# Performance work log

Hardware: AMD Instinct MI355X
Metric: run time of the kernel (lower is better)

## Reference

```python
import jax, jax.numpy as jnp
import numpy as np
import math

POWER = 4
NUM_LEVELS = 2
STDS = [8, 4, 2, 1]          # stds sorted descending, as in __init__
KSIZE = 31                    # max(stds)*4 - 1
MAX_MIP = (NUM_LEVELS - 1) + math.log(2 * max(STDS)) / math.log(POWER)  # 3.0


def _blur_kernel():
    # (12, 3, 31, 31): output channel 3*i+c is a Gaussian(std=STDS[i]) applied to input channel c
    d = np.arange(KSIZE, dtype=np.float64) - (KSIZE - 1) / 2.0
    K = np.zeros((3 * len(STDS), 3, KSIZE, KSIZE), np.float32)
    for i, s in enumerate(STDS):
        g1 = np.exp(-0.5 * (d / s) ** 2)
        g1 = g1 / g1.sum()
        g = np.outer(g1, g1).astype(np.float32)
        for c in range(3):
            K[3 * i + c, c] = g
    return jnp.asarray(K)


def cube_sample(tex, dirs):
    # tex: (6, H, W, 3) cubemap faces in OpenGL order (+x,-x,+y,-y,+z,-z); dirs: (B, 3)
    H, W = tex.shape[1], tex.shape[2]
    x, y, z = dirs[:, 0], dirs[:, 1], dirs[:, 2]
    ax, ay, az = jnp.abs(x), jnp.abs(y), jnp.abs(z)
    is_x = (ax >= ay) & (ax >= az)
    is_y = (~is_x) & (ay >= az)
    face = jnp.where(is_x, jnp.where(x >= 0, 0, 1),
                     jnp.where(is_y, jnp.where(y >= 0, 2, 3),
                               jnp.where(z >= 0, 4, 5)))
    ma = jnp.where(is_x, ax, jnp.where(is_y, ay, az))
    conds = [face == i for i in range(6)]
    sc = jnp.select(conds, [-z, z, x, x, x, -x])
    tc = jnp.select(conds, [-y, -y, z, -z, -y, -y])
    inv = 1.0 / jnp.maximum(ma, 1e-12)
    u = 0.5 * (sc * inv + 1.0)
    v = 0.5 * (tc * inv + 1.0)
    fx = u * W - 0.5
    fy = v * H - 0.5
    x0 = jnp.floor(fx)
    y0 = jnp.floor(fy)
    wx = (fx - x0)[:, None]
    wy = (fy - y0)[:, None]
    x0i = jnp.clip(x0, 0, W - 1).astype(jnp.int32)
    x1i = jnp.clip(x0 + 1, 0, W - 1).astype(jnp.int32)
    y0i = jnp.clip(y0, 0, H - 1).astype(jnp.int32)
    y1i = jnp.clip(y0 + 1, 0, H - 1).astype(jnp.int32)
    t00 = tex[face, y0i, x0i]
    t10 = tex[face, y0i, x1i]
    t01 = tex[face, y1i, x0i]
    t11 = tex[face, y1i, x1i]
    return ((t00 * (1 - wx) + t10 * wx) * (1 - wy)
            + (t01 * (1 - wx) + t11 * wx) * wy)


def setup_inputs() -> dict:
    key = jax.random.key(0)
    k1, k2, k3, k4 = jax.random.split(key, 4)
    B = 2097152
    res = 512
    viewdirs = jax.random.normal(k1, (B, 3), dtype=jnp.float32)
    viewdirs = viewdirs / jnp.linalg.norm(viewdirs, axis=-1, keepdims=True)
    # miplevel = log(saSample/saTexel)/log(4)/2 ; make it span [0, 3.2] so the mask path fires
    saTexel = 4.0 * math.pi / (6 * res * res)
    u = jax.random.uniform(k2, (B, 1), dtype=jnp.float32)
    saSample = saTexel * (float(POWER) ** (2.0 * 3.2 * u))
    # learned cubemaps: coarse (128) then fine (512), as in bg_mats list order
    bg_mat0 = 0.1 + 0.05 * jax.random.normal(k3, (6, 128, 128, 3), dtype=jnp.float32)
    bg_mat1 = 0.1 + 0.05 * jax.random.normal(k4, (6, 512, 512, 3), dtype=jnp.float32)
    return {"viewdirs": viewdirs, "saSample": saSample, "bg_mat0": bg_mat0, "bg_mat1": bg_mat1}


def reference(viewdirs, saSample, bg_mat0, bg_mat1):
    res = bg_mat1.shape[1]
    saTexel = 4.0 * math.pi / (6 * res * res)
    miplevel = jnp.clip(jnp.log(saSample / saTexel) / math.log(POWER) / 2.0, 0.0, MAX_MIP)  # (B,1)

    # main level pass: mip=1 (coarse, weight 1/(2-1)=1), mip=0 (fine, weight 1/2)
    img = cube_sample(bg_mat0, viewdirs) * 1.0 + cube_sample(bg_mat1, viewdirs) * 0.5

    # blur pyramid from coarse map (start_mip=1, weight=1, identity activation)
    faces = jnp.transpose(bg_mat0, (0, 3, 1, 2))  # (6,3,h,h)
    conv = jax.lax.conv_general_dilated(faces, _blur_kernel(), (1, 1), 'SAME',
                                        dimension_numbers=('NCHW', 'OIHW', 'NCHW'))
    blur = jnp.zeros_like(img)
    wsum = jnp.zeros_like(miplevel)
    for i, s in enumerate(STDS):
        mat = jnp.transpose(conv[:, 3 * i:3 * i + 3], (0, 2, 3, 1))  # (6,h,h,3)
        mip = (NUM_LEVELS - 1) + math.log(2 * s) / math.log(POWER)
        w = 1.0 - jnp.clip(jnp.abs(mip - miplevel), 0.0, 1.0)  # (B,1)
        blur = blur + cube_sample(mat, viewdirs) * w
        wsum = wsum + w
    mask = miplevel >= NUM_LEVELS  # (B,1)
    img = jnp.where(mask, blur / jnp.maximum(wsum, 1e-8), img)
    return img
```

## Files before the change

kernel.cpp:

```cpp
#include <hip/hip_runtime.h>
#include <hip/hip_fp16.h>
#include <math.h>

#define KSIZE 31
#define HRAD 15

#define QSCALE (1023.0f / 0.75f)
#define QINV   (0.75f / 1023.0f)
#define QOFF   0.25f

union H8U { float4 f4; __half h[8]; };

__device__ inline unsigned quant3(float r, float g, float b) {
    int qr = (int)((r + QOFF) * QSCALE + 0.5f);
    int qg = (int)((g + QOFF) * QSCALE + 0.5f);
    int qb = (int)((b + QOFF) * QSCALE + 0.5f);
    qr = min(max(qr, 0), 1023);
    qg = min(max(qg, 0), 1023);
    qb = min(max(qb, 0), 1023);
    return (unsigned)(qr | (qg << 10) | (qb << 20));
}

__device__ inline float deqc(unsigned q, int sh) {
    return (float)((q >> sh) & 1023u) * QINV - QOFF;
}

__device__ inline void cube_coords(float x, float y, float z,
                                   int& face, float& u, float& v) {
    float ax = fabsf(x), ay = fabsf(y), az = fabsf(z);
    bool is_x = (ax >= ay) && (ax >= az);
    bool is_y = (!is_x) && (ay >= az);
    float ma, sc, tc;
    if (is_x) {
        if (x >= 0.0f) { face = 0; sc = -z; } else { face = 1; sc = z; }
        ma = ax; tc = -y;
    } else if (is_y) {
        if (y >= 0.0f) { face = 2; tc = z; } else { face = 3; tc = -z; }
        ma = ay; sc = x;
    } else {
        if (z >= 0.0f) { face = 4; sc = x; } else { face = 5; sc = -x; }
        ma = az; tc = -y;
    }
    float inv = 1.0f / fmaxf(ma, 1e-12f);
    u = 0.5f * (sc * inv + 1.0f);
    v = 0.5f * (tc * inv + 1.0f);
}

__device__ inline void nbq_setup(float u, float v, int HW, int face,
                                 int& rec, float& wx, float& wy) {
    float fx = u * (float)HW - 0.5f;
    float fy = v * (float)HW - 0.5f;
    float x0 = floorf(fx), y0 = floorf(fy);
    wx = fx - x0;
    wy = fy - y0;
    int xi = (int)x0, yi = (int)y0;
    if (xi < 0) { xi = 0; wx = 0.0f; }
    if (yi < 0) { yi = 0; wy = 0.0f; }
    rec = (face * HW + yi) * HW + xi;
}

__device__ inline void weights_inline(int tid, float wS[4][32]) {
    const float ss[4] = {8.f, 4.f, 2.f, 1.f};
    int lvl = (tid >> 5) & 3;
    int tap = tid & 31;
    float d = (float)tap - 15.0f;
    float q = d / ss[lvl];
    float g = (tap < KSIZE) ? expf(-0.5f * q * q) : 0.0f;
    float s = g;
#pragma unroll
    for (int k = 16; k; k >>= 1) s += __shfl_xor(s, k, 32);
    if (tid < 128) wS[lvl][tap] = g / s;
}

__global__ __launch_bounds__(256)
void hblur(const float* __restrict__ bg0, float4* __restrict__ tmpH,
           uint4* __restrict__ bg0q) {
    __shared__ float sm[1664];
    float (*rows)[2][384] = (float (*)[2][384])sm;
    float (*wS)[32] = (float (*)[32])(sm + 1536);

    int bid  = blockIdx.x;
    int tid  = threadIdx.x;
    int unit = tid >> 7;
    int lane = tid & 127;
    int face = bid / 64;
    int yrow = (bid % 64) * 2 + unit;

    weights_inline(tid, wS);

    int ynext = min(yrow + 1, 127);
    const float* srcA = bg0 + (size_t)(face * 128 + yrow) * 384;
    const float* srcB = bg0 + (size_t)(face * 128 + ynext) * 384;
    for (int k = lane; k < 384; k += 128) {
        rows[unit][0][k] = srcA[k];
        rows[unit][1][k] = srcB[k];
    }
    __syncthreads();

    int x = lane;
    float a[4][3] = {};
    for (int t = 0; t < KSIZE; ++t) {
        int xx = x + t - HRAD;
        if (xx >= 0 && xx < 128) {
            float r0 = rows[unit][0][xx * 3 + 0];
            float r1 = rows[unit][0][xx * 3 + 1];
            float r2 = rows[unit][0][xx * 3 + 2];
#pragma unroll
            for (int l = 0; l < 4; ++l) {
                float w = wS[l][t];
                a[l][0] += w * r0; a[l][1] += w * r1; a[l][2] += w * r2;
            }
        }
    }
    size_t idx = (size_t)(face * 128 + yrow) * 128 + x;
    H8U ta, tb;
#pragma unroll
    for (int l = 0; l < 2; ++l) {
        ta.h[l * 4 + 0] = __float2half(a[l][0]);
        ta.h[l * 4 + 1] = __float2half(a[l][1]);
        ta.h[l * 4 + 2] = __float2half(a[l][2]);
        ta.h[l * 4 + 3] = __float2half(0.0f);
        tb.h[l * 4 + 0] = __float2half(a[2 + l][0]);
        tb.h[l * 4 + 1] = __float2half(a[2 + l][1]);
        tb.h[l * 4 + 2] = __float2half(a[2 + l][2]);
        tb.h[l * 4 + 3] = __float2half(0.0f);
    }
    tmpH[idx * 2 + 0] = ta.f4;
    tmpH[idx * 2 + 1] = tb.f4;

    int x1 = min(x + 1, 127);
    uint4 r;
    r.x = quant3(rows[unit][0][x * 3 + 0], rows[unit][0][x * 3 + 1], rows[unit][0][x * 3 + 2]);
    r.y = quant3(rows[unit][0][x1 * 3 + 0], rows[unit][0][x1 * 3 + 1], rows[unit][0][x1 * 3 + 2]);
    r.z = quant3(rows[unit][1][x * 3 + 0], rows[unit][1][x * 3 + 1], rows[unit][1][x * 3 + 2]);
    r.w = quant3(rows[unit][1][x1 * 3 + 0], rows[unit][1][x1 * 3 + 1], rows[unit][1][x1 * 3 + 2]);
    bg0q[idx] = r;
}

__global__ __launch_bounds__(256)
void packv(const float* __restrict__ bg1, const float4* __restrict__ tmpH,
           uint4* __restrict__ bg1q, uint2* __restrict__ blurq2) {
    __shared__ float4 sm4[768];
    int b = blockIdx.x;
    int tid = threadIdx.x;

    if (b < 3072) {
        float* sm = (float*)sm4;
        int y    = b & 511;
        int face = b >> 9;
        int yn   = min(y + 1, 511);
        const float4* rA = (const float4*)(bg1 + (size_t)(face * 512 + y)  * 1536);
        const float4* rB = (const float4*)(bg1 + (size_t)(face * 512 + yn) * 1536);
        for (int i = tid; i < 384; i += 256) {
            sm4[i]       = rA[i];
            sm4[384 + i] = rB[i];
        }
        __syncthreads();
        const float* a  = sm;
        const float* bb = sm + 1536;
#pragma unroll
        for (int e = 0; e < 2; ++e) {
            int x  = e * 256 + tid;
            int x1 = min(x + 1, 511);
            uint4 r;
            r.x = quant3(a[x * 3 + 0],  a[x * 3 + 1],  a[x * 3 + 2]);
            r.y = quant3(a[x1 * 3 + 0], a[x1 * 3 + 1], a[x1 * 3 + 2]);
            r.z = quant3(bb[x * 3 + 0],  bb[x * 3 + 1],  bb[x * 3 + 2]);
            r.w = quant3(bb[x1 * 3 + 0], bb[x1 * 3 + 1], bb[x1 * 3 + 2]);
            bg1q[(size_t)(face * 512 + y) * 512 + x] = r;
        }
        return;
    }

    float (*wS)[32] = (float (*)[32])sm4;
    int bb   = b - 3072;
    int yrow = bb & 127;
    int face = bb >> 7;

    weights_inline(tid, wS);
    __syncthreads();

    int x    = tid >> 1;
    int half = tid & 1;
    float a0 = 0.f, a1 = 0.f, a2 = 0.f, a3 = 0.f, a4 = 0.f, a5 = 0.f;
    int ylo = max(yrow - HRAD, 0);
    int yhi = min(yrow + HRAD, 127);
    for (int yy = ylo; yy <= yhi; ++yy) {
        int t = yy - yrow + HRAD;
        H8U q;
        q.f4 = tmpH[((size_t)(face * 128 + yy) * 128 + x) * 2 + half];
        float wA = wS[half * 2 + 0][t];
        float wB = wS[half * 2 + 1][t];
        a0 += wA * __half2float(q.h[0]);
        a1 += wA * __half2float(q.h[1]);
        a2 += wA * __half2float(q.h[2]);
        a3 += wB * __half2float(q.h[4]);
        a4 += wB * __half2float(q.h[5]);
        a5 += wB * __half2float(q.h[6]);
    }
    uint2 o;
    o.x = quant3(a0, a1, a2);
    o.y = quant3(a3, a4, a5);
    blurq2[((size_t)(face * 128 + yrow) * 128 + x) * 2 + half] = o;
}

__device__ inline void shade_one(float x, float y, float z, float sa,
                                 const uint4* __restrict__ bg0q,
                                 const uint4* __restrict__ bg1q,
                                 const uint4* __restrict__ blurq,
                                 float* __restrict__ R) {
    int face; float u, v;
    cube_coords(x, y, z, face, u, v);

    const float saTexel = (float)(4.0 * M_PI / (6.0 * 512.0 * 512.0));
    float m = logf(sa / saTexel);
    m = m / 1.3862943611198906f;
    m = m * 0.5f;
    m = fminf(fmaxf(m, 0.0f), 3.0f);

    if (m >= 2.0f) {
        float fx = u * 128.0f - 0.5f;
        float fy = v * 128.0f - 0.5f;
        float xf = floorf(fx), yf = floorf(fy);
        float wx = fx - xf, wy = fy - yf;
        int x0i = min(max((int)xf, 0), 127);
        int x1i = min(max((int)xf + 1, 0), 127);
        int y0i = min(max((int)yf, 0), 127);
        int y1i = min(max((int)yf + 1, 0), 127);
        int base = face << 14;
        uint4 q00 = blurq[base + y0i * 128 + x0i];
        uint4 q10 = blurq[base + y0i * 128 + x1i];
        uint4 q01 = blurq[base + y1i * 128 + x0i];
        uint4 q11 = blurq[base + y1i * 128 + x1i];

        float w0 = 1.0f - fminf(fabsf(3.0f - m), 1.0f);
        float w1 = 1.0f - fminf(fabsf(2.5f - m), 1.0f);
        float w2 = 1.0f - fminf(fabsf(2.0f - m), 1.0f);
        float w3 = 1.0f - fminf(fabsf(1.5f - m), 1.0f);
        float inv = 1.0f / fmaxf(w0 + w1 + w2 + w3, 1e-8f);

#pragma unroll
        for (int c = 0; c < 3; ++c) {
            int sh = c * 10;
            float v00 = w0 * deqc(q00.x, sh) + w1 * deqc(q00.y, sh) +
                        w2 * deqc(q00.z, sh) + w3 * deqc(q00.w, sh);
            float v10 = w0 * deqc(q10.x, sh) + w1 * deqc(q10.y, sh) +
                        w2 * deqc(q10.z, sh) + w3 * deqc(q10.w, sh);
            float v01 = w0 * deqc(q01.x, sh) + w1 * deqc(q01.y, sh) +
                        w2 * deqc(q01.z, sh) + w3 * deqc(q01.w, sh);
            float v11 = w0 * deqc(q11.x, sh) + w1 * deqc(q11.y, sh) +
                        w2 * deqc(q11.z, sh) + w3 * deqc(q11.w, sh);
            float top = v00 * (1.0f - wx) + v10 * wx;
            float bot = v01 * (1.0f - wx) + v11 * wx;
            R[c] = (top * (1.0f - wy) + bot * wy) * inv;
        }
    } else {
        int r0; float wx0, wy0;
        nbq_setup(u, v, 128, face, r0, wx0, wy0);
        int r1; float wx1, wy1;
        nbq_setup(u, v, 512, face, r1, wx1, wy1);
        uint4 p0 = bg0q[r0];
        uint4 p1 = bg1q[r1];
#pragma unroll
        for (int c = 0; c < 3; ++c) {
            int sh = c * 10;
            float t0 = deqc(p0.x, sh) * (1.0f - wx0) + deqc(p0.y, sh) * wx0;
            float b0 = deqc(p0.z, sh) * (1.0f - wx0) + deqc(p0.w, sh) * wx0;
            float c0 = t0 * (1.0f - wy0) + b0 * wy0;
            float t1 = deqc(p1.x, sh) * (1.0f - wx1) + deqc(p1.y, sh) * wx1;
            float b1 = deqc(p1.z, sh) * (1.0f - wx1) + deqc(p1.w, sh) * wx1;
            float c1 = t1 * (1.0f - wy1) + b1 * wy1;
            R[c] = c0 + 0.5f * c1;
        }
    }
}

__global__ __launch_bounds__(256)
void shade4(const float4* __restrict__ vd4, const float4* __restrict__ sa4,
            const uint4* __restrict__ bg0q, const uint4* __restrict__ bg1q,
            const uint4* __restrict__ blurq, float4* __restrict__ out4,
            int nquads) {
    int q = blockIdx.x * blockDim.x + threadIdx.x;
    if (q >= nquads) return;

    float4 a = vd4[3 * q + 0];
    float4 b = vd4[3 * q + 1];
    float4 c = vd4[3 * q + 2];
    float4 s = sa4[q];

    float X[4] = {a.x, a.w, b.z, c.y};
    float Y[4] = {a.y, b.x, b.w, c.z};
    float Z[4] = {a.z, b.y, c.x, c.w};
    float S[4] = {s.x, s.y, s.z, s.w};

    float R[12];
#pragma unroll
    for (int r = 0; r < 4; ++r) {
        shade_one(X[r], Y[r], Z[r], S[r], bg0q, bg1q, blurq, &R[3 * r]);
    }

    out4[3 * q + 0] = make_float4(R[0], R[1], R[2],  R[3]);
    out4[3 * q + 1] = make_float4(R[4], R[5], R[6],  R[7]);
    out4[3 * q + 2] = make_float4(R[8], R[9], R[10], R[11]);
}

extern "C" void kernel_launch(void* const* d_in, const int* in_sizes, int n_in,
                              void* d_out, int out_size, void* d_ws, size_t ws_size,
                              hipStream_t stream) {
    const float* viewdirs = (const float*)d_in[0];
    const float* saSample = (const float*)d_in[1];
    const float* bg0      = (const float*)d_in[2];
    const float* bg1      = (const float*)d_in[3];
    float* out = (float*)d_out;

    int B = in_sizes[0] / 3;
    int nquads = B / 4;

    uint4*  blurq = (uint4*)d_ws;
    uint4*  bg0q  = blurq + 98304;
    uint4*  bg1q  = bg0q + 98304;
    float4* tmpH  = (float4*)(bg1q + 1572864);

    hblur<<<384, 256, 0, stream>>>(bg0, tmpH, bg0q);
    packv<<<3072 + 768, 256, 0, stream>>>(bg1, tmpH, bg1q, (uint2*)blurq);

    int blocks = (nquads + 255) / 256;
    shade4<<<blocks, 256, 0, stream>>>((const float4*)viewdirs,
                                       (const float4*)saSample,
                                       bg0q, bg1q, blurq,
                                       (float4*)out, nquads);
}
```

Measured before the change: 80.45 us.

## Move bg1 quantization into first prep kernel, tile 8 rows per block

The fine-map (bg1) quantize/pack work moves from the second pre-pass kernel into the first, running alongside the horizontal blur blocks. It is also retiled so each block handles 8 output rows from 9 staged input rows instead of one row from two. This cuts redundant row loads and block count, and the second kernel now runs only the vertical blur with smaller shared memory. The cost is a larger shared-memory footprint (about 55KB) in the first kernel, which may limit occupancy.

```diff
diff --git a/kernel.cpp b/kernel.cpp
--- a/kernel.cpp
+++ b/kernel.cpp
@@ -73,14 +73,47 @@
 }
 
 __global__ __launch_bounds__(256)
-void hblur(const float* __restrict__ bg0, float4* __restrict__ tmpH,
-           uint4* __restrict__ bg0q) {
-    __shared__ float sm[1664];
+void prep1(const float* __restrict__ bg0, const float* __restrict__ bg1,
+           float4* __restrict__ tmpH, uint4* __restrict__ bg0q,
+           uint4* __restrict__ bg1q) {
+    __shared__ float4 sm4[3456];
+    float* sm = (float*)sm4;
+    int b = blockIdx.x;
+    int tid = threadIdx.x;
+
+    if (b < 384) {
+        int face  = b / 64;
+        int ytile = (b % 64) * 8;
+        for (int i = tid; i < 9 * 384; i += 256) {
+            int r  = i / 384;
+            int c4 = i - r * 384;
+            int gy = min(ytile + r, 511);
+            sm4[r * 384 + c4] =
+                ((const float4*)(bg1 + (size_t)(face * 512 + gy) * 1536))[c4];
+        }
+        __syncthreads();
+#pragma unroll
+        for (int i = 0; i < 16; ++i) {
+            int idx = i * 256 + tid;
+            int yl  = idx >> 9;
+            int x   = idx & 511;
+            int x1  = min(x + 1, 511);
+            const float* rA = sm + (size_t)yl * 1536;
+            const float* rB = sm + (size_t)(yl + 1) * 1536;
+            uint4 r;
+            r.x = quant3(rA[x * 3 + 0],  rA[x * 3 + 1],  rA[x * 3 + 2]);
+            r.y = quant3(rA[x1 * 3 + 0], rA[x1 * 3 + 1], rA[x1 * 3 + 2]);
+            r.z = quant3(rB[x * 3 + 0],  rB[x * 3 + 1],  rB[x * 3 + 2]);
+            r.w = quant3(rB[x1 * 3 + 0], rB[x1 * 3 + 1], rB[x1 * 3 + 2]);
+            bg1q[(size_t)(face * 512 + ytile + yl) * 512 + x] = r;
+        }
+        return;
+    }
+
     float (*rows)[2][384] = (float (*)[2][384])sm;
     float (*wS)[32] = (float (*)[32])(sm + 1536);
 
-    int bid  = blockIdx.x;
-    int tid  = threadIdx.x;
+    int bid  = b - 384;
     int unit = tid >> 7;
     int lane = tid & 127;
     int face = bid / 64;
@@ -138,44 +171,12 @@
 }
 
 __global__ __launch_bounds__(256)
-void packv(const float* __restrict__ bg1, const float4* __restrict__ tmpH,
-           uint4* __restrict__ bg1q, uint2* __restrict__ blurq2) {
-    __shared__ float4 sm4[768];
-    int b = blockIdx.x;
-    int tid = threadIdx.x;
-
-    if (b < 3072) {
-        float* sm = (float*)sm4;
-        int y    = b & 511;
-        int face = b >> 9;
-        int yn   = min(y + 1, 511);
-        const float4* rA = (const float4*)(bg1 + (size_t)(face * 512 + y)  * 1536);
-        const float4* rB = (const float4*)(bg1 + (size_t)(face * 512 + yn) * 1536);
-        for (int i = tid; i < 384; i += 256) {
-            sm4[i]       = rA[i];
-            sm4[384 + i] = rB[i];
-        }
-        __syncthreads();
-        const float* a  = sm;
-        const float* bb = sm + 1536;
-#pragma unroll
-        for (int e = 0; e < 2; ++e) {
-            int x  = e * 256 + tid;
-            int x1 = min(x + 1, 511);
-            uint4 r;
-            r.x = quant3(a[x * 3 + 0],  a[x * 3 + 1],  a[x * 3 + 2]);
-            r.y = quant3(a[x1 * 3 + 0], a[x1 * 3 + 1], a[x1 * 3 + 2]);
-            r.z = quant3(bb[x * 3 + 0],  bb[x * 3 + 1],  bb[x * 3 + 2]);
-            r.w = quant3(bb[x1 * 3 + 0], bb[x1 * 3 + 1], bb[x1 * 3 + 2]);
-            bg1q[(size_t)(face * 512 + y) * 512 + x] = r;
-        }
-        return;
-    }
-
-    float (*wS)[32] = (float (*)[32])sm4;
-    int bb   = b - 3072;
-    int yrow = bb & 127;
-    int face = bb >> 7;
+void vblur(const float4* __restrict__ tmpH, uint2* __restrict__ blurq2) {
+    __shared__ float wS[4][32];
+    int b    = blockIdx.x;
+    int tid  = threadIdx.x;
+    int yrow = b & 127;
+    int face = b >> 7;
 
     weights_inline(tid, wS);
     __syncthreads();
@@ -321,8 +322,8 @@
     uint4*  bg1q  = bg0q + 98304;
     float4* tmpH  = (float4*)(bg1q + 1572864);
 
-    hblur<<<384, 256, 0, stream>>>(bg0, tmpH, bg0q);
-    packv<<<3072 + 768, 256, 0, stream>>>(bg1, tmpH, bg1q, (uint2*)blurq);
+    prep1<<<768, 256, 0, stream>>>(bg0, bg1, tmpH, bg0q, bg1q);
+    vblur<<<768, 256, 0, stream>>>(tmpH, (uint2*)blurq);
 
     int blocks = (nquads + 255) / 256;
     shade4<<<blocks, 256, 0, stream>>>((const float4*)viewdirs,
```

Result: faster. 78.12 us (median of 2 runs) (-2.9%).
